# Kernel optimization log

Measured on AMD Instinct MI355X. Metric: run time of the kernel, lower is better.

The kernel has to match this reference:

```python
import jax, jax.numpy as jnp
import numpy as np

B, H, W, C = 16, 96, 96, 128
FOCAL_LEVEL = 3
FOCAL_WINDOW = 3
FOCAL_FACTOR = 2
LN_EPS = 1e-3  # keras LayerNormalization default epsilon


def dwconv_same(x, k):
    # x: [B,H,W,C], k: [kh,kw,1,C] depthwise kernel (feature_group_count=C)
    return jax.lax.conv_general_dilated(
        x, k, window_strides=(1, 1), padding='SAME',
        dimension_numbers=('NHWC', 'HWIO', 'NHWC'),
        feature_group_count=x.shape[-1])


def setup_inputs() -> dict:
    key = jax.random.key(0)
    ks = jax.random.split(key, 12)
    s = 0.02
    out_f = 2 * C + (FOCAL_LEVEL + 1)
    inp = {
        'x': jax.random.normal(ks[0], (B, H, W, C), dtype=jnp.float32),
        'Wf': jax.random.normal(ks[1], (C, out_f), dtype=jnp.float32) * s,
        'bf': jnp.zeros((out_f,), dtype=jnp.float32),
        'Wh': jax.random.normal(ks[2], (C, C), dtype=jnp.float32) * s,
        'bh': jnp.zeros((C,), dtype=jnp.float32),
        'gamma': jnp.ones((C,), dtype=jnp.float32),
        'beta': jnp.zeros((C,), dtype=jnp.float32),
        'Wp': jax.random.normal(ks[3], (C, C), dtype=jnp.float32) * s,
        'bp': jnp.zeros((C,), dtype=jnp.float32),
    }
    for l in range(FOCAL_LEVEL):
        kk = FOCAL_FACTOR * l + FOCAL_WINDOW  # 3, 5, 7
        inp[f'k{l}'] = jax.random.normal(ks[4 + l], (kk, kk, 1, C), dtype=jnp.float32) * s
    return inp


def reference(x, Wf, bf, k0, k1, k2, Wh, bh, gamma, beta, Wp, bp):
    gelu = lambda t: jax.nn.gelu(t, approximate=False)  # keras gelu is exact
    y = jnp.einsum('bhwc,cd->bhwd', x, Wf) + bf  # f(): [B,H,W,2C+L+1]
    q = y[..., :C]
    ctx = y[..., C:2 * C]
    gates = y[..., 2 * C:]  # [B,H,W,L+1]

    ctx_all = jnp.zeros_like(ctx)
    for l, k in enumerate((k0, k1, k2)):
        ctx = gelu(dwconv_same(ctx, k))
        ctx_all = ctx_all + ctx * gates[..., l:l + 1]

    ctx_global = gelu(jnp.mean(ctx, axis=(1, 2), keepdims=True))  # [B,1,1,C]
    ctx_all = ctx_all + ctx_global * gates[..., FOCAL_LEVEL:]

    modulator = jnp.einsum('bhwc,cd->bhwd', ctx_all, Wh) + bh  # 1x1 conv h()
    x_out = q * modulator

    # post-LN over channel dim
    mu = jnp.mean(x_out, axis=-1, keepdims=True)
    var = jnp.mean(jnp.square(x_out - mu), axis=-1, keepdims=True)
    x_out = (x_out - mu) * jax.lax.rsqrt(var + LN_EPS) * gamma + beta

    x_out = jnp.einsum('bhwc,cd->bhwd', x_out, Wp) + bp  # proj (dropout p=0)
    return x_out
```

## Files before the change

### kernel.cpp

```cpp
#include <hip/hip_runtime.h>
#include <math.h>

#define B_ 16
#define H_ 96
#define W_ 96
#define C_ 128
#define HW_ (H_*W_)
#define NTOK (B_*HW_)
#define NOUT 260

#define TH 16
#define TW 32
#define B0H 28
#define B0W 44
#define B1H 26
#define B1W 42
#define B2H 22
#define B2W 38

typedef unsigned short ushort_t;
typedef unsigned int uint_t;
typedef float f32x4 __attribute__((ext_vector_type(4)));
typedef float f32x2 __attribute__((ext_vector_type(2)));
typedef short bfrag __attribute__((ext_vector_type(8)));
typedef unsigned short us8 __attribute__((ext_vector_type(8)));

__device__ __forceinline__ float gelu_f(float t) {
    const float x  = t * 0.7071067811865475f;
    const float ax = fabsf(x);
    const float u  = __fdividef(1.0f, fmaf(0.3275911f, ax, 1.0f));
    float p = fmaf(1.061405429f, u, -1.453152027f);
    p = fmaf(p, u, 1.421413741f);
    p = fmaf(p, u, -0.284496736f);
    p = fmaf(p, u, 0.254829592f);
    p = p * u;
    const float e  = __expf(-ax * ax);
    float er = fmaf(-p, e, 1.0f);
    er = (x < 0.0f) ? -er : er;
    return 0.5f * t * (1.0f + er);
}
__device__ __forceinline__ float b2f(ushort_t u) {
    union { unsigned int i; float f; } t; t.i = (unsigned int)u << 16; return t.f;
}
__device__ __forceinline__ ushort_t f2b(float f) {
    union { float f; unsigned int i; } t; t.f = f;
    unsigned int lsb = (t.i >> 16) & 1u;
    t.i += 0x7fffu + lsb;
    return (ushort_t)(t.i >> 16);
}
__device__ __forceinline__ void unp2(uint_t u, float& a, float& b) {
    union { unsigned int i; float f; } x, y;
    x.i = u << 16; y.i = u & 0xffff0000u;
    a = x.f; b = y.f;
}
__device__ __forceinline__ void unp8(const uint4 v, float* f) {
    unp2(v.x, f[0], f[1]); unp2(v.y, f[2], f[3]);
    unp2(v.z, f[4], f[5]); unp2(v.w, f[6], f[7]);
}
__device__ __forceinline__ uint_t pk2(float a, float b) {
    return (uint_t)f2b(a) | ((uint_t)f2b(b) << 16);
}
__device__ __forceinline__ uint4 pk8(const float* f) {
    uint4 v;
    v.x = pk2(f[0], f[1]); v.y = pk2(f[2], f[3]);
    v.z = pk2(f[4], f[5]); v.w = pk2(f[6], f[7]);
    return v;
}
__device__ __forceinline__ f32x2 unp2p(uint_t u) {
    union { uint_t i; float f; } a, b;
    a.i = u << 16; b.i = u & 0xffff0000u;
    f32x2 r; r.x = a.f; r.y = b.f; return r;
}
__device__ __forceinline__ void unp8p(const uint4 v, f32x2* d) {
    d[0] = unp2p(v.x); d[1] = unp2p(v.y); d[2] = unp2p(v.z); d[3] = unp2p(v.w);
}

__device__ __forceinline__ void split8_to(const float* f,
                                          ushort_t* __restrict__ hdst,
                                          ushort_t* __restrict__ ldst) {
    us8 vh, vl;
    #pragma unroll
    for (int j = 0; j < 8; ++j) {
        const ushort_t h = f2b(f[j]);
        vh[j] = h;
        vl[j] = f2b(f[j] - b2f(h));
    }
    *(us8*)hdst = vh;
    *(us8*)ldst = vl;
}

__global__ __launch_bounds__(128) void pack_weights(
    const float* __restrict__ Wf, const float* __restrict__ Wh,
    const float* __restrict__ Wp, ushort_t* __restrict__ pk)
{
    const int n = blockIdx.x, mat = blockIdx.y, k = threadIdx.x;
    if (mat == 4 && n >= 16) return;
    float v;
    if (mat == 0)      v = Wf[(size_t)k * NOUT + n];
    else if (mat == 1) v = Wf[(size_t)k * NOUT + C_ + n];
    else if (mat == 2) v = Wh[(size_t)k * C_ + n];
    else if (mat == 3) v = Wp[(size_t)k * C_ + n];
    else               v = (n < 4) ? Wf[(size_t)k * NOUT + 2*C_ + n] : 0.0f;
    const ushort_t h = f2b(v);
    const ushort_t l = f2b(v - b2f(h));
    ushort_t* base = pk + (size_t)mat * (2 * C_ * C_);
    const int lo_off = (mat == 4) ? 16 * C_ : C_ * C_;
    base[n * C_ + k] = h;
    base[lo_off + n * C_ + k] = l;
}

template <bool A_LO>
__device__ __forceinline__ void mfma_gemm64(
    const ushort_t (*Ah)[136], const ushort_t (*Al)[136],
    const ushort_t* __restrict__ Bh, const ushort_t* __restrict__ Bl,
    int lane, int n0, f32x4 acc[4][2])
{
    const int ar = lane & 15;
    const int ak = (lane >> 4) << 3;
    #pragma unroll
    for (int kk = 0; kk < 4; ++kk) {
        const int kb = (kk << 5) + ak;
        const bfrag bh0 = *(const bfrag*)(Bh + (((n0      + ar) << 7) + kb));
        const bfrag bh1 = *(const bfrag*)(Bh + (((n0 + 16 + ar) << 7) + kb));
        const bfrag bl0 = *(const bfrag*)(Bl + (((n0      + ar) << 7) + kb));
        const bfrag bl1 = *(const bfrag*)(Bl + (((n0 + 16 + ar) << 7) + kb));
        #pragma unroll
        for (int m = 0; m < 4; ++m) {
            const bfrag ah = *(const bfrag*)&Ah[(m << 4) + ar][kb];
            if constexpr (A_LO) {
                const bfrag al = *(const bfrag*)&Al[(m << 4) + ar][kb];
                acc[m][0] = __builtin_amdgcn_mfma_f32_16x16x32_bf16(al, bh0, acc[m][0], 0, 0, 0);
                acc[m][1] = __builtin_amdgcn_mfma_f32_16x16x32_bf16(al, bh1, acc[m][1], 0, 0, 0);
            }
            acc[m][0] = __builtin_amdgcn_mfma_f32_16x16x32_bf16(ah, bl0, acc[m][0], 0, 0, 0);
            acc[m][1] = __builtin_amdgcn_mfma_f32_16x16x32_bf16(ah, bl1, acc[m][1], 0, 0, 0);
            acc[m][0] = __builtin_amdgcn_mfma_f32_16x16x32_bf16(ah, bh0, acc[m][0], 0, 0, 0);
            acc[m][1] = __builtin_amdgcn_mfma_f32_16x16x32_bf16(ah, bh1, acc[m][1], 0, 0, 0);
        }
    }
}

__device__ __forceinline__ void stage_split_f32(
    const float* __restrict__ src, int tid,
    ushort_t (*Ah)[136], ushort_t (*Al)[136])
{
    #pragma unroll
    for (int p = 0; p < 4; ++p) {
        const int i  = tid + (p << 8);
        const int t  = i >> 4;
        const int c8 = (i & 15) << 3;
        const float4 v0 = *(const float4*)(src + (size_t)t * C_ + c8);
        const float4 v1 = *(const float4*)(src + (size_t)t * C_ + c8 + 4);
        const float f[8] = {v0.x, v0.y, v0.z, v0.w, v1.x, v1.y, v1.z, v1.w};
        split8_to(f, &Ah[t][c8], &Al[t][c8]);
    }
}

__global__ __launch_bounds__(256) void gemm_ctx_gates_mfma(
    const float* __restrict__ x, const float* __restrict__ bf,
    const ushort_t* __restrict__ pk,
    ushort_t* __restrict__ ctx, float* __restrict__ gates,
    float* __restrict__ csum)
{
    __shared__ ushort_t Abuf[2][64][136];
    const int tid  = threadIdx.x;
    const int tok0 = blockIdx.x * 64;
    const int lane = tid & 63;
    const int n0   = (tid >> 6) << 5;

    if (blockIdx.x < 8) csum[blockIdx.x * 256 + tid] = 0.0f;

    stage_split_f32(x + (size_t)tok0 * C_, tid, Abuf[0], Abuf[1]);
    __syncthreads();

    f32x4 acc[4][2] = {};
    {
        const ushort_t* Bh = pk + (size_t)1 * (2 * C_ * C_);
        const ushort_t* Bl = Bh + C_ * C_;
        mfma_gemm64<true>(Abuf[0], Abuf[1], Bh, Bl, lane, n0, acc);
    }

    {
        const int w  = tid >> 6;
        const int ar = lane & 15;
        const int ak = (lane >> 4) << 3;
        const ushort_t* Gh = pk + (size_t)4 * (2 * C_ * C_);
        const ushort_t* Gl = Gh + 16 * C_;
        f32x4 gacc = {};
        #pragma unroll
        for (int kk = 0; kk < 4; ++kk) {
            const int kb = (kk << 5) + ak;
            const bfrag gh = *(const bfrag*)(Gh + ((ar << 7) + kb));
            const bfrag gl = *(const bfrag*)(Gl + ((ar << 7) + kb));
            const bfrag ah = *(const bfrag*)&Abuf[0][(w << 4) + ar][kb];
            const bfrag al = *(const bfrag*)&Abuf[1][(w << 4) + ar][kb];
            gacc = __builtin_amdgcn_mfma_f32_16x16x32_bf16(al, gh, gacc, 0, 0, 0);
            gacc = __builtin_amdgcn_mfma_f32_16x16x32_bf16(ah, gl, gacc, 0, 0, 0);
            gacc = __builtin_amdgcn_mfma_f32_16x16x32_bf16(ah, gh, gacc, 0, 0, 0);
        }
        if (ar < 4) {
            const int rg = (lane >> 4) << 2;
            #pragma unroll
            for (int r = 0; r < 4; ++r)
                gates[(size_t)(tok0 + (w << 4) + rg + r) * 4 + ar] = gacc[r] + bf[2*C_ + ar];
        }
    }
    __syncthreads();

    {
        const int ar = lane & 15;
        const int rg = (lane >> 4) << 2;
        #pragma unroll
        for (int n = 0; n < 2; ++n) {
            const int col = n0 + (n << 4) + ar;
            const float bias = bf[C_ + col];
            #pragma unroll
            for (int m = 0; m < 4; ++m)
                #pragma unroll
                for (int r = 0; r < 4; ++r)
                    Abuf[0][(m << 4) + rg + r][col] = f2b(acc[m][n][r] + bias);
        }
    }
    __syncthreads();

    #pragma unroll
    for (int p = 0; p < 4; ++p) {
        const int i  = tid + (p << 8);
        const int cg = i >> 6;
        const int t  = i & 63;
        *(uint4*)(ctx + (((size_t)cg * NTOK + tok0 + t) << 3))
            = *(const uint4*)&Abuf[0][t][cg << 3];
    }
}

__global__ __launch_bounds__(256, 4) void focal_conv_fused(
    const ushort_t* __restrict__ ctx_in,
    const float* __restrict__ k0w, const float* __restrict__ k1w,
    const float* __restrict__ k2w,
    const float* __restrict__ gates,
    ushort_t* __restrict__ ctx_all,
    float* __restrict__ csum)
{
    __shared__ uint4 bufA[B0H*B0W];
    __shared__ uint4 buf1[B1H*B1W];
    __shared__ float wts[(9+25+49)*8];

    const int tid  = threadIdx.x;
    const int cg   = blockIdx.x;
    const int tile = blockIdx.y;
    const int bb   = blockIdx.z;
    const int wt   = tile % 3, ht = tile / 3;
    const int c0   = cg << 3;
    const int h0   = ht * TH, w0 = wt * TW;

    if (tid < 166) {
        const int f = tid << 2;
        const float* src; int r;
        if (f < 72)       { r = f;       src = k0w; }
        else if (f < 272) { r = f - 72;  src = k1w; }
        else              { r = f - 272; src = k2w; }
        const int tap = r >> 3, off = r & 7;
        *(float4*)&wts[f] = *(const float4*)(src + tap * C_ + c0 + off);
    }

    const ushort_t* cin = ctx_in + (((size_t)cg * NTOK + (size_t)bb * HW_) << 3);
    for (int i = tid; i < B0H*B0W; i += 256) {
        const int r = i / B0W, q = i - r * B0W;
        const int hh = h0 - 6 + r, ww = w0 - 6 + q;
        uint4 v = make_uint4(0u, 0u, 0u, 0u);
        if ((unsigned)hh < (unsigned)H_ && (unsigned)ww < (unsigned)W_)
            v = *(const uint4*)(cin + ((size_t)(hh * W_ + ww) << 3));
        bufA[i] = v;
    }
    __syncthreads();

    {
        int iv[5], ecp[5], boff[5];
        #pragma unroll
        for (int p = 0; p < 5; ++p) {
            const int e = tid + (p << 8);
            iv[p] = (e < B1H*B1W);
            const int ec = iv[p] ? e : 0;
            ecp[p] = ec;
            boff[p] = (ec / B1W) * B0W + (ec % B1W);
        }
        f32x2 acc[5][4] = {};
        #pragma unroll 1
        for (int a = 0; a < 3; ++a) {
            #pragma unroll
            for (int b = 0; b < 3; ++b) {
                f32x2 wv[4];
                #pragma unroll
                for (int c = 0; c < 4; ++c)
                    wv[c] = *(const f32x2*)&wts[(a*3+b)*8 + 2*c];
                const int off = a * B0W + b;
                #pragma unroll
                for (int p = 0; p < 5; ++p) {
                    f32x2 d[4]; unp8p(bufA[boff[p] + off], d);
                    #pragma unroll
                    for (int c = 0; c < 4; ++c)
                        acc[p][c] = __builtin_elementwise_fma(d[c], wv[c], acc[p][c]);
                }
            }
        }
        __syncthreads();
        #pragma unroll
        for (int p = 0; p < 5; ++p) if (iv[p]) {
            float g[8];
            #pragma unroll
            for (int c = 0; c < 4; ++c) {
                g[2*c]   = gelu_f(acc[p][c].x);
                g[2*c+1] = gelu_f(acc[p][c].y);
            }
            buf1[ecp[p]] = pk8(g);
        }
    }
    __syncthreads();

    {
        int iv[4], ecp[4], boff[4];
        #pragma unroll
        for (int p = 0; p < 4; ++p) {
            const int e = tid + (p << 8);
            iv[p] = (e < B2H*B2W);
            const int ec = iv[p] ? e : 0;
            ecp[p] = ec;
            boff[p] = (ec / B2W) * B1W + (ec % B2W);
        }
        f32x2 acc[4][4] = {};
        #pragma unroll 1
        for (int a = 0; a < 5; ++a) {
            #pragma unroll
            for (int b = 0; b < 5; ++b) {
                f32x2 wv[4];
                #pragma unroll
                for (int c = 0; c < 4; ++c)
                    wv[c] = *(const f32x2*)&wts[72 + (a*5+b)*8 + 2*c];
                const int off = a * B1W + b;
                #pragma unroll
                for (int p = 0; p < 4; ++p) {
                    f32x2 d[4]; unp8p(buf1[boff[p] + off], d);
                    #pragma unroll
                    for (int c = 0; c < 4; ++c)
                        acc[p][c] = __builtin_elementwise_fma(d[c], wv[c], acc[p][c]);
                }
            }
        }
        __syncthreads();
        #pragma unroll
        for (int p = 0; p < 4; ++p) if (iv[p]) {
            float g[8];
            #pragma unroll
            for (int c = 0; c < 4; ++c) {
                g[2*c]   = gelu_f(acc[p][c].x);
                g[2*c+1] = gelu_f(acc[p][c].y);
            }
            bufA[ecp[p]] = pk8(g);
        }
    }
    __syncthreads();

    float lsum[8] = {};
    {
        const int th0 = tid >> 5, tw0 = tid & 31;
        f32x2 acc[2][4] = {};
        #pragma unroll 1
        for (int a = 0; a < 7; ++a) {
            #pragma unroll
            for (int b = 0; b < 7; ++b) {
                f32x2 wv[4];
                #pragma unroll
                for (int c = 0; c < 4; ++c)
                    wv[c] = *(const f32x2*)&wts[272 + (a*7+b)*8 + 2*c];
                #pragma unroll
                for (int p = 0; p < 2; ++p) {
                    const int th = th0 + (p << 3);
                    f32x2 d[4]; unp8p(bufA[(th + a)*B2W + (tw0 + b)], d);
                    #pragma unroll
                    for (int c = 0; c < 4; ++c)
                        acc[p][c] = __builtin_elementwise_fma(d[c], wv[c], acc[p][c]);
                }
            }
        }
        #pragma unroll
        for (int p = 0; p < 2; ++p) {
            const int th = th0 + (p << 3);
            float ctx3[8];
            #pragma unroll
            for (int c = 0; c < 4; ++c) {
                ctx3[2*c]   = gelu_f(acc[p][c].x);
                ctx3[2*c+1] = gelu_f(acc[p][c].y);
            }
            #pragma unroll
            for (int c = 0; c < 8; ++c) lsum[c] += ctx3[c];
            float d1[8]; unp8(buf1[(5+th)*B1W + (5+tw0)], d1);
            float d2[8]; unp8(bufA[(th+3)*B2W + (tw0+3)], d2);
            const size_t pix = (size_t)bb * HW_ + (size_t)(h0 + th) * W_ + (w0 + tw0);
            const float4 gt = *(const float4*)(gates + pix * 4);
            float o[8];
            #pragma unroll
            for (int c = 0; c < 8; ++c)
                o[c] = d1[c] * gt.x + d2[c] * gt.y + ctx3[c] * gt.z;
            *(uint4*)(ctx_all + pix * C_ + c0) = pk8(o);
        }
    }

    __syncthreads();
    float* red = (float*)bufA;
    #pragma unroll
    for (int c = 0; c < 8; ++c) red[c*256 + tid] = lsum[c];
    __syncthreads();
    for (int off = 128; off > 0; off >>= 1) {
        if (tid < off) {
            #pragma unroll
            for (int c = 0; c < 8; ++c)
                red[c*256 + tid] += red[c*256 + tid + off];
        }
        __syncthreads();
    }
    if (tid < 8) atomicAdd(&csum[bb * C_ + c0 + tid], red[tid * 256]);
}

__global__ __launch_bounds__(128) void glob_mod(
    const float* __restrict__ csum, const float* __restrict__ Wh,
    float* __restrict__ whc)
{
    __shared__ float cg[128];
    const int b = blockIdx.x, n = threadIdx.x;
    cg[n] = gelu_f(csum[b * C_ + n] * (1.0f / (float)HW_));
    __syncthreads();
    float s = 0.f;
    #pragma unroll 8
    for (int k = 0; k < C_; ++k)
        s = fmaf(cg[k], Wh[(size_t)k * C_ + n], s);
    whc[b * C_ + n] = s;
}

__global__ __launch_bounds__(256) void modq_ln_out_mfma(
    const ushort_t* __restrict__ ctx_all, const float* __restrict__ whc,
    const float* __restrict__ gates, const float* __restrict__ x,
    const ushort_t* __restrict__ pk, const float* __restrict__ bf,
    const float* __restrict__ bh, const float* __restrict__ gamma,
    const float* __restrict__ beta, const float* __restrict__ bp,
    float* __restrict__ out)
{
    __shared__ ushort_t Abuf[2][64][136];
    __shared__ float g3s[64];
    __shared__ float whcs[128];
    __shared__ float mu_s[64];
    __shared__ float rs_s[64];
    float (*xs)[132] = (float(*)[132])&Abuf[0][0][0];
    ushort_t (*xlnb)[136] = (ushort_t(*)[136])&Abuf[0][0][0];

    const int tid  = threadIdx.x;
    const int tok0 = blockIdx.x * 64;
    const int bidx = tok0 / HW_;
    const int lane = tid & 63;
    const int n0   = (tid >> 6) << 5;
    const int ar   = lane & 15;
    const int rg   = (lane >> 4) << 2;

    #pragma unroll
    for (int p = 0; p < 4; ++p) {
        const int i  = tid + (p << 8);
        const int t  = i >> 4;
        const int c8 = (i & 15) << 3;
        *(us8*)&Abuf[0][t][c8] = *(const us8*)(ctx_all + (size_t)(tok0 + t) * C_ + c8);
    }
    if (tid < 64)           g3s[tid]        = gates[(size_t)(tok0 + tid) * 4 + 3];
    else if (tid < 192)     whcs[tid - 64]  = whc[bidx * C_ + (tid - 64)];
    __syncthreads();

    f32x4 am[4][2] = {};
    {
        const ushort_t* Bh2 = pk + (size_t)2 * (2 * C_ * C_);
        const ushort_t* Bl2 = Bh2 + C_ * C_;
        mfma_gemm64<false>(Abuf[0], Abuf[0], Bh2, Bl2, lane, n0, am);
    }
    __syncthreads();

    stage_split_f32(x + (size_t)tok0 * C_, tid, Abuf[0], Abuf[1]);
    __syncthreads();

    f32x4 aq[4][2] = {};
    {
        const ushort_t* Bh0 = pk;
        const ushort_t* Bl0 = Bh0 + C_ * C_;
        mfma_gemm64<true>(Abuf[0], Abuf[1], Bh0, Bl0, lane, n0, aq);
    }
    __syncthreads();

    {
        #pragma unroll
        for (int n = 0; n < 2; ++n) {
            const int col = n0 + (n << 4) + ar;
            const float bfv = bf[col];
            const float bhv = bh[col];
            const float whv = whcs[col];
            #pragma unroll
            for (int m = 0; m < 4; ++m)
                #pragma unroll
                for (int r = 0; r < 4; ++r) {
                    const int row = (m << 4) + rg + r;
                    const float mod = am[m][n][r] + g3s[row] * whv + bhv;
                    xs[row][col] = (aq[m][n][r] + bfv) * mod;
                }
        }
    }
    __syncthreads();

    if (tid < 64) {
        float s = 0.f, s2 = 0.f;
        #pragma unroll
        for (int c = 0; c < C_; c += 4) {
            const float4 v = *(const float4*)&xs[tid][c];
            s  += v.x + v.y + v.z + v.w;
            s2 += v.x*v.x + v.y*v.y + v.z*v.z + v.w*v.w;
        }
        const float mu  = s * (1.0f / 128.0f);
        const float var = s2 * (1.0f / 128.0f) - mu * mu;
        mu_s[tid] = mu;
        rs_s[tid] = rsqrtf(var + 0.001f);
    }
    __syncthreads();

    {
        const int tt = tid >> 2;
        const int c0b = (tid & 3) << 5;
        const float mu = mu_s[tt], rs = rs_s[tt];
        uint_t xw[16];
        #pragma unroll
        for (int j = 0; j < 8; ++j) {
            const int c = c0b + (j << 2);
            const float4 v  = *(const float4*)&xs[tt][c];
            const float4 gm = *(const float4*)(gamma + c);
            const float4 bt = *(const float4*)(beta + c);
            xw[2*j]   = pk2((v.x - mu) * rs * gm.x + bt.x,
                            (v.y - mu) * rs * gm.y + bt.y);
            xw[2*j+1] = pk2((v.z - mu) * rs * gm.z + bt.z,
                            (v.w - mu) * rs * gm.w + bt.w);
        }
        __syncthreads();
        #pragma unroll
        for (int j = 0; j < 4; ++j)
            *(uint4*)&xlnb[tt][c0b + (j << 3)] = *(uint4*)&xw[4*j];
    }
    __syncthreads();

    f32x4 ao[4][2] = {};
    {
        const ushort_t* Bh3 = pk + (size_t)3 * (2 * C_ * C_);
        const ushort_t* Bl3 = Bh3 + C_ * C_;
        mfma_gemm64<false>((const ushort_t(*)[136])xlnb,
                           (const ushort_t(*)[136])xlnb, Bh3, Bl3, lane, n0, ao);
    }
    {
        #pragma unroll
        for (int n = 0; n < 2; ++n) {
            const int col = n0 + (n << 4) + ar;
            const float bpv = bp[col];
            #pragma unroll
            for (int m = 0; m < 4; ++m)
                #pragma unroll
                for (int r = 0; r < 4; ++r) {
                    const int row = (m << 4) + rg + r;
                    out[(size_t)(tok0 + row) * C_ + col] = ao[m][n][r] + bpv;
                }
        }
    }
}

extern "C" void kernel_launch(void* const* d_in, const int* in_sizes, int n_in,
                              void* d_out, int out_size, void* d_ws, size_t ws_size,
                              hipStream_t stream) {
    const float* x     = (const float*)d_in[0];
    const float* Wf    = (const float*)d_in[1];
    const float* bf    = (const float*)d_in[2];
    const float* Wh    = (const float*)d_in[3];
    const float* bh    = (const float*)d_in[4];
    const float* gamma = (const float*)d_in[5];
    const float* beta  = (const float*)d_in[6];
    const float* Wp    = (const float*)d_in[7];
    const float* bp    = (const float*)d_in[8];
    const float* k0    = (const float*)d_in[9];
    const float* k1    = (const float*)d_in[10];
    const float* k2    = (const float*)d_in[11];
    float* out = (float*)d_out;

    const size_t NC = (size_t)NTOK * C_;
    ushort_t* P0  = (ushort_t*)d_ws;
    ushort_t* ACC = P0 + NC;
    float* gates  = (float*)(ACC + NC);
    float* csum   = gates + (size_t)NTOK * 4;
    float* whc    = csum + (size_t)B_ * C_;
    ushort_t* pkw = (ushort_t*)(whc + (size_t)B_ * C_);

    pack_weights<<<dim3(C_, 5), 128, 0, stream>>>(Wf, Wh, Wp, pkw);
    gemm_ctx_gates_mfma<<<NTOK / 64, 256, 0, stream>>>(x, bf, pkw, P0, gates, csum);
    focal_conv_fused<<<dim3(C_/8, (H_/TH)*(W_/TW), B_), 256, 0, stream>>>(
        P0, k0, k1, k2, gates, ACC, csum);
    glob_mod<<<B_, 128, 0, stream>>>(csum, Wh, whc);
    modq_ln_out_mfma<<<NTOK / 64, 256, 0, stream>>>(
        ACC, whc, gates, x, pkw, bf, bh, gamma, beta, bp, out);
}
```

Measured before the change: 453.1 us.

## Use hardware bf16 pack conversion, erff GELU, and parallelize LayerNorm statistics

```diff
diff --git a/kernel.cpp b/kernel.cpp
--- a/kernel.cpp
+++ b/kernel.cpp
@@ -26,18 +26,7 @@
 typedef unsigned short us8 __attribute__((ext_vector_type(8)));
 
 __device__ __forceinline__ float gelu_f(float t) {
-    const float x  = t * 0.7071067811865475f;
-    const float ax = fabsf(x);
-    const float u  = __fdividef(1.0f, fmaf(0.3275911f, ax, 1.0f));
-    float p = fmaf(1.061405429f, u, -1.453152027f);
-    p = fmaf(p, u, 1.421413741f);
-    p = fmaf(p, u, -0.284496736f);
-    p = fmaf(p, u, 0.254829592f);
-    p = p * u;
-    const float e  = __expf(-ax * ax);
-    float er = fmaf(-p, e, 1.0f);
-    er = (x < 0.0f) ? -er : er;
-    return 0.5f * t * (1.0f + er);
+    return 0.5f * t * (1.0f + erff(t * 0.7071067811865475f));
 }
 __device__ __forceinline__ float b2f(ushort_t u) {
     union { unsigned int i; float f; } t; t.i = (unsigned int)u << 16; return t.f;
@@ -48,6 +37,11 @@
     t.i += 0x7fffu + lsb;
     return (ushort_t)(t.i >> 16);
 }
+__device__ __forceinline__ uint_t pk2(float a, float b) {
+    uint_t r;
+    asm("v_cvt_pk_bf16_f32 %0, %1, %2" : "=v"(r) : "v"(a), "v"(b));
+    return r;
+}
 __device__ __forceinline__ void unp2(uint_t u, float& a, float& b) {
     union { unsigned int i; float f; } x, y;
     x.i = u << 16; y.i = u & 0xffff0000u;
@@ -56,9 +50,6 @@
 __device__ __forceinline__ void unp8(const uint4 v, float* f) {
     unp2(v.x, f[0], f[1]); unp2(v.y, f[2], f[3]);
     unp2(v.z, f[4], f[5]); unp2(v.w, f[6], f[7]);
-}
-__device__ __forceinline__ uint_t pk2(float a, float b) {
-    return (uint_t)f2b(a) | ((uint_t)f2b(b) << 16);
 }
 __device__ __forceinline__ uint4 pk8(const float* f) {
     uint4 v;
@@ -78,15 +69,18 @@
 __device__ __forceinline__ void split8_to(const float* f,
                                           ushort_t* __restrict__ hdst,
                                           ushort_t* __restrict__ ldst) {
-    us8 vh, vl;
+    uint_t hp[4], lp[4];
     #pragma unroll
-    for (int j = 0; j < 8; ++j) {
-        const ushort_t h = f2b(f[j]);
-        vh[j] = h;
-        vl[j] = f2b(f[j] - b2f(h));
-    }
-    *(us8*)hdst = vh;
-    *(us8*)ldst = vl;
+    for (int j = 0; j < 4; ++j) {
+        const float a = f[2*j], b = f[2*j+1];
+        const uint_t h = pk2(a, b);
+        union { uint_t i; float f; } ha, hb;
+        ha.i = h << 16; hb.i = h & 0xffff0000u;
+        hp[j] = h;
+        lp[j] = pk2(a - ha.f, b - hb.f);
+    }
+    *(uint4*)hdst = make_uint4(hp[0], hp[1], hp[2], hp[3]);
+    *(uint4*)ldst = make_uint4(lp[0], lp[1], lp[2], lp[3]);
 }
 
 __global__ __launch_bounds__(128) void pack_weights(
@@ -215,10 +209,15 @@
             const int col = n0 + (n << 4) + ar;
             const float bias = bf[C_ + col];
             #pragma unroll
-            for (int m = 0; m < 4; ++m)
-                #pragma unroll
-                for (int r = 0; r < 4; ++r)
-                    Abuf[0][(m << 4) + rg + r][col] = f2b(acc[m][n][r] + bias);
+            for (int m = 0; m < 4; ++m) {
+                const int rowb = (m << 4) + rg;
+                const uint_t p0 = pk2(acc[m][n][0] + bias, acc[m][n][1] + bias);
+                const uint_t p1 = pk2(acc[m][n][2] + bias, acc[m][n][3] + bias);
+                Abuf[0][rowb + 0][col] = (ushort_t)p0;
+                Abuf[0][rowb + 1][col] = (ushort_t)(p0 >> 16);
+                Abuf[0][rowb + 2][col] = (ushort_t)p1;
+                Abuf[0][rowb + 3][col] = (ushort_t)(p1 >> 16);
+            }
         }
     }
     __syncthreads();
@@ -449,6 +448,7 @@
     __shared__ float whcs[128];
     __shared__ float mu_s[64];
     __shared__ float rs_s[64];
+    __shared__ f32x2 part[64][4];
     float (*xs)[132] = (float(*)[132])&Abuf[0][0][0];
     ushort_t (*xlnb)[136] = (ushort_t(*)[136])&Abuf[0][0][0];
 
@@ -509,14 +509,25 @@
     }
     __syncthreads();
 
-    if (tid < 64) {
+    {
+        const int tt = tid >> 2;
+        const int qq = tid & 3;
         float s = 0.f, s2 = 0.f;
         #pragma unroll
-        for (int c = 0; c < C_; c += 4) {
-            const float4 v = *(const float4*)&xs[tid][c];
+        for (int c = 0; c < 32; c += 4) {
+            const float4 v = *(const float4*)&xs[tt][(qq << 5) + c];
             s  += v.x + v.y + v.z + v.w;
             s2 += v.x*v.x + v.y*v.y + v.z*v.z + v.w*v.w;
         }
+        f32x2 pr; pr.x = s; pr.y = s2;
+        part[tt][qq] = pr;
+    }
+    __syncthreads();
+    if (tid < 64) {
+        const f32x2 p0 = part[tid][0], p1 = part[tid][1];
+        const f32x2 p2 = part[tid][2], p3 = part[tid][3];
+        const float s  = (p0.x + p1.x) + (p2.x + p3.x);
+        const float s2 = (p0.y + p1.y) + (p2.y + p3.y);
         const float mu  = s * (1.0f / 128.0f);
         const float var = s2 * (1.0f / 128.0f) - mu * mu;
         mu_s[tid] = mu;
```

After: 405.7 us. 1.12x faster.
